# Performance work log

Hardware: AMD Instinct MI355X
Metric: run time of the kernel (lower is better)

Reference implementation:

```python
import jax, jax.numpy as jnp
import numpy as np

B, IN_DIM, D, P = 256, 1024, 512, 2048


def setup_inputs() -> dict:
    key = jax.random.key(0)
    ks = jax.random.split(key, 7)
    return {
        "x": jax.random.normal(ks[0], (B, IN_DIM), dtype=jnp.float32),
        "y": jax.random.randint(ks[1], (B,), 0, P),
        "Wb": jax.random.normal(ks[2], (D, IN_DIM), dtype=jnp.float32) * 0.02,
        "bb": jax.random.normal(ks[3], (D,), dtype=jnp.float32) * 0.02,
        "Wm": jax.random.normal(ks[4], (P, D), dtype=jnp.float32) * 0.02,
        "bm": jax.random.normal(ks[5], (P,), dtype=jnp.float32) * 0.02,
        "proxies": jax.random.normal(ks[6], (P, D), dtype=jnp.float32),
    }


def reference(x, y, Wb, bb, Wm, bm, proxies):
    # backbone: Linear(in_dim -> D)
    feat = x @ Wb.T + bb                         # [B, D]
    # L2-norm regularizer: mean of per-row L2 norms
    reg_e = jnp.mean(jnp.sqrt(jnp.sum(feat * feat, axis=1)))
    # multi: classification head Linear(D -> P)
    out = feat @ Wm.T + bm                       # [B, P]
    # squared euclidean distance to each proxy (broadcast diff + square + sum)
    den = jnp.sum((feat[:, None, :] - proxies[None, :, :]) ** 2, axis=2)  # [B, P]
    # cross-entropy on negated distances
    logp = jax.nn.log_softmax(-den, axis=1)      # [B, P]
    loss = -jnp.mean(jnp.take_along_axis(logp, y[:, None], axis=1))
    return out, loss, reg_e
```

## Files before the change

### kernel.cpp

```cpp
#include <hip/hip_runtime.h>
#include <hip/hip_bf16.h>
#include <math.h>

#define NB   256
#define KIN  1024
#define ND   512
#define NP   2048
#define NTOT 4096

typedef __bf16 bf16x8 __attribute__((ext_vector_type(8)));
typedef float  f32x4  __attribute__((ext_vector_type(4)));
typedef unsigned short ush8 __attribute__((ext_vector_type(8)));

#define OFF_WPB    0u
#define OFF_FEAT32 4194304u
#define OFF_PN2    4718592u
#define OFF_LOGITS 4726784u
#define OFF_ROWLP  6823936u
#define OFF_ROWNM  6824960u

__device__ __forceinline__ ush8 pack8(float4 f0, float4 f1) {
    union { ush8 v; __hip_bfloat162 h[4]; } o;
    o.h[0] = __float22bfloat162_rn(make_float2(f0.x, f0.y));
    o.h[1] = __float22bfloat162_rn(make_float2(f0.z, f0.w));
    o.h[2] = __float22bfloat162_rn(make_float2(f1.x, f1.y));
    o.h[3] = __float22bfloat162_rn(make_float2(f1.z, f1.w));
    return o.v;
}
__device__ __forceinline__ float4 add4(float4 a, float4 b) {
    return make_float4(a.x + b.x, a.y + b.y, a.z + b.z, a.w + b.w);
}

__global__ __launch_bounds__(256) void k_prep(
    const float* __restrict__ Wm, const float* __restrict__ prox,
    unsigned short* __restrict__ WPb, float* __restrict__ pn2,
    float* __restrict__ feat32)
{
    const int t = threadIdx.x, lane = t & 63, w = t >> 6;
    if (t < 128) feat32[blockIdx.x * 128 + t] = 0.f;
    const int r = blockIdx.x * 4 + w;
    const float* src = (r < NP) ? (Wm + (size_t)r * ND)
                                : (prox + (size_t)(r - NP) * ND);
    float4 v0 = *(const float4*)(src + lane * 8);
    float4 v1 = *(const float4*)(src + lane * 8 + 4);
    *(ush8*)(WPb + (size_t)r * ND + lane * 8) = pack8(v0, v1);
    if (r >= NP) {
        float s = v0.x*v0.x + v0.y*v0.y + v0.z*v0.z + v0.w*v0.w
                + v1.x*v1.x + v1.y*v1.y + v1.z*v1.z + v1.w*v1.w;
#pragma unroll
        for (int off = 32; off; off >>= 1) s += __shfl_down(s, off);
        if (lane == 0) pn2[r - NP] = s;
    }
}

__global__ __launch_bounds__(256) void k_feat(
    const float* __restrict__ x, const float* __restrict__ Wb,
    float* __restrict__ feat32)
{
    __shared__ unsigned short As[2][64 * 32];
    __shared__ unsigned short Bs[2][64 * 32];
    const int t = threadIdx.x, lane = t & 63, w = t >> 6;
    const int n0 = blockIdx.x * 64, m0 = blockIdx.y * 64, k0 = blockIdx.z * 128;
    const int srow = t >> 2, sc = (t & 3) * 8;
    const float* gA = x  + (size_t)(m0 + srow) * KIN + k0 + sc;
    const float* gB = Wb + (size_t)(n0 + srow) * KIN + k0 + sc;
    float4 a0 = *(const float4*)gA, a1 = *(const float4*)(gA + 4);
    float4 b0 = *(const float4*)gB, b1 = *(const float4*)(gB + 4);
    f32x4 acc[2][2] = {};
    const int wm = (w >> 1) * 32, wn = (w & 1) * 32;
    const int arow = wm + (lane & 15), brow = wn + (lane & 15);
    const int fcol = (lane >> 4) * 8;
#pragma unroll
    for (int ks = 0; ks < 4; ++ks) {
        *(ush8*)&As[ks & 1][srow * 32 + sc] = pack8(a0, a1);
        *(ush8*)&Bs[ks & 1][srow * 32 + sc] = pack8(b0, b1);
        __syncthreads();
        if (ks + 1 < 4) {
            a0 = *(const float4*)(gA + (ks + 1) * 32);
            a1 = *(const float4*)(gA + (ks + 1) * 32 + 4);
            b0 = *(const float4*)(gB + (ks + 1) * 32);
            b1 = *(const float4*)(gB + (ks + 1) * 32 + 4);
        }
        const unsigned short* as = &As[ks & 1][0];
        const unsigned short* bs = &Bs[ks & 1][0];
        bf16x8 af0 = *(const bf16x8*)&as[(arow     ) * 32 + fcol];
        bf16x8 af1 = *(const bf16x8*)&as[(arow + 16) * 32 + fcol];
        bf16x8 bf0 = *(const bf16x8*)&bs[(brow     ) * 32 + fcol];
        bf16x8 bf1 = *(const bf16x8*)&bs[(brow + 16) * 32 + fcol];
        acc[0][0] = __builtin_amdgcn_mfma_f32_16x16x32_bf16(af0, bf0, acc[0][0], 0, 0, 0);
        acc[0][1] = __builtin_amdgcn_mfma_f32_16x16x32_bf16(af0, bf1, acc[0][1], 0, 0, 0);
        acc[1][0] = __builtin_amdgcn_mfma_f32_16x16x32_bf16(af1, bf0, acc[1][0], 0, 0, 0);
        acc[1][1] = __builtin_amdgcn_mfma_f32_16x16x32_bf16(af1, bf1, acc[1][1], 0, 0, 0);
    }
    const int q = lane >> 4, cn = lane & 15;
#pragma unroll
    for (int i = 0; i < 2; ++i)
#pragma unroll
        for (int j = 0; j < 2; ++j) {
            const int n = n0 + wn + 16 * j + cn;
#pragma unroll
            for (int r = 0; r < 4; ++r) {
                const int m = m0 + wm + 16 * i + q * 4 + r;
                atomicAdd(&feat32[m * ND + n], acc[i][j][r]);
            }
        }
}

__global__ __launch_bounds__(256) void k_head(
    const float* __restrict__ feat32, const float* __restrict__ bb,
    const unsigned short* __restrict__ WPb,
    const float* __restrict__ bm, const float* __restrict__ pn2,
    float* __restrict__ out, float* __restrict__ logits)
{
    __shared__ unsigned short As[2][64 * 32];
    __shared__ unsigned short Bs[2][64 * 32];
    const int t = threadIdx.x, lane = t & 63, w = t >> 6;
    const int n0 = blockIdx.x * 64;
    const int m0 = blockIdx.y * 64;
    const int srow = t >> 2, sc = (t & 3) * 8;
    const float*          gA = feat32 + (size_t)(m0 + srow) * ND + sc;
    const unsigned short* gB = WPb    + (size_t)(n0 + srow) * ND + sc;
    float4 a0 = *(const float4*)gA, a1 = *(const float4*)(gA + 4);
    float4 u0 = *(const float4*)(bb + sc), u1 = *(const float4*)(bb + sc + 4);
    ush8 vb = *(const ush8*)gB;
    f32x4 acc[2][2] = {};
    const int wm = (w >> 1) * 32, wn = (w & 1) * 32;
    const int fr = lane & 15, fcol = (lane >> 4) * 8;
    for (int ks = 0; ks < ND / 32; ++ks) {
        *(ush8*)&As[ks & 1][srow * 32 + sc] = pack8(add4(a0, u0), add4(a1, u1));
        *(ush8*)&Bs[ks & 1][srow * 32 + sc] = vb;
        __syncthreads();
        if (ks + 1 < ND / 32) {
            a0 = *(const float4*)(gA + (ks + 1) * 32);
            a1 = *(const float4*)(gA + (ks + 1) * 32 + 4);
            u0 = *(const float4*)(bb + (ks + 1) * 32 + sc);
            u1 = *(const float4*)(bb + (ks + 1) * 32 + sc + 4);
            vb = *(const ush8*)(gB + (ks + 1) * 32);
        }
        const unsigned short* as = &As[ks & 1][0];
        const unsigned short* bs = &Bs[ks & 1][0];
        bf16x8 af0 = *(const bf16x8*)&as[(wm      + fr) * 32 + fcol];
        bf16x8 af1 = *(const bf16x8*)&as[(wm + 16 + fr) * 32 + fcol];
        bf16x8 bf0 = *(const bf16x8*)&bs[(wn      + fr) * 32 + fcol];
        bf16x8 bf1 = *(const bf16x8*)&bs[(wn + 16 + fr) * 32 + fcol];
        acc[0][0] = __builtin_amdgcn_mfma_f32_16x16x32_bf16(af0, bf0, acc[0][0], 0, 0, 0);
        acc[0][1] = __builtin_amdgcn_mfma_f32_16x16x32_bf16(af0, bf1, acc[0][1], 0, 0, 0);
        acc[1][0] = __builtin_amdgcn_mfma_f32_16x16x32_bf16(af1, bf0, acc[1][0], 0, 0, 0);
        acc[1][1] = __builtin_amdgcn_mfma_f32_16x16x32_bf16(af1, bf1, acc[1][1], 0, 0, 0);
    }
    const bool isProxy = (n0 >= NP);
    const int q = lane >> 4;
#pragma unroll
    for (int i = 0; i < 2; ++i)
#pragma unroll
        for (int j = 0; j < 2; ++j) {
            const int n = n0 + wn + 16 * j + fr;
            const float cadd = isProxy ? pn2[n - NP] : bm[n];
#pragma unroll
            for (int r = 0; r < 4; ++r) {
                const int m = m0 + wm + 16 * i + q * 4 + r;
                const float v = acc[i][j][r];
                if (isProxy) logits[m * NP + (n - NP)] = 2.0f * v - cadd;
                else         out[m * NP + n] = v + cadd;
            }
        }
}

__device__ __forceinline__ float block_reduce(float v, float* sred, int op)
{
    const int lane = threadIdx.x & 63, wave = threadIdx.x >> 6;
#pragma unroll
    for (int off = 32; off; off >>= 1) {
        float o = __shfl_down(v, off);
        v = op ? fmaxf(v, o) : (v + o);
    }
    if (lane == 0) sred[wave] = v;
    __syncthreads();
    if (threadIdx.x == 0) {
        float r = sred[0];
#pragma unroll
        for (int wv = 1; wv < 4; ++wv) r = op ? fmaxf(r, sred[wv]) : (r + sred[wv]);
        sred[0] = r;
    }
    __syncthreads();
    float r = sred[0];
    __syncthreads();
    return r;
}

__global__ __launch_bounds__(256) void k_loss(
    const float* __restrict__ feat32, const float* __restrict__ bb,
    const float* __restrict__ logits, const int* __restrict__ y,
    float* __restrict__ rowlp, float* __restrict__ rownm)
{
    __shared__ float sred[4];
    const int b = blockIdx.x, t = threadIdx.x;

    float v0 = feat32[b * ND + t] + bb[t];
    float v1 = feat32[b * ND + t + 256] + bb[t + 256];
    float fn2 = block_reduce(v0 * v0 + v1 * v1, sred, 0);

    const float* lr = logits + (size_t)b * NP;
    float lv[8], mx = -INFINITY;
#pragma unroll
    for (int j = 0; j < 8; ++j) { lv[j] = lr[t + 256 * j]; mx = fmaxf(mx, lv[j]); }
    float MX = block_reduce(mx, sred, 1);
    float es = 0.f;
#pragma unroll
    for (int j = 0; j < 8; ++j) es += __expf(lv[j] - MX);
    float SUM = block_reduce(es, sred, 0);

    if (t == 0) {
        float ly = lr[y[b]];
        rowlp[b] = ly - MX - __logf(SUM);
        rownm[b] = sqrtf(fn2);
    }
}

__global__ __launch_bounds__(256) void k_final(
    const float* __restrict__ rowlp, const float* __restrict__ rownm,
    float* __restrict__ tail)
{
    __shared__ float sred[4];
    const int t = threadIdx.x;
    float s1 = block_reduce(rowlp[t], sred, 0);
    float s2 = block_reduce(rownm[t], sred, 0);
    if (t == 0) {
        tail[0] = -s1 / (float)NB;
        tail[1] =  s2 / (float)NB;
    }
}

extern "C" void kernel_launch(void* const* d_in, const int* in_sizes, int n_in,
                              void* d_out, int out_size, void* d_ws, size_t ws_size,
                              hipStream_t stream)
{
    const float* x       = (const float*)d_in[0];
    const int*   y       = (const int*)  d_in[1];
    const float* Wb      = (const float*)d_in[2];
    const float* bb      = (const float*)d_in[3];
    const float* Wm      = (const float*)d_in[4];
    const float* bm      = (const float*)d_in[5];
    const float* proxies = (const float*)d_in[6];

    char* ws = (char*)d_ws;
    unsigned short* WPb    = (unsigned short*)(ws + OFF_WPB);
    float*          feat32 = (float*)(ws + OFF_FEAT32);
    float*          pn2    = (float*)(ws + OFF_PN2);
    float*          logits = (float*)(ws + OFF_LOGITS);
    float*          rowlp  = (float*)(ws + OFF_ROWLP);
    float*          rownm  = (float*)(ws + OFF_ROWNM);

    float* out  = (float*)d_out;
    float* tail = out + (size_t)NB * NP;

    k_prep <<<dim3(NTOT / 4), dim3(256), 0, stream>>>(Wm, proxies, WPb, pn2, feat32);
    k_feat <<<dim3(ND / 64, NB / 64, 8), dim3(256), 0, stream>>>(x, Wb, feat32);
    k_head <<<dim3(NTOT / 64, NB / 64), dim3(256), 0, stream>>>(
        feat32, bb, WPb, bm, pn2, out, logits);
    k_loss <<<dim3(NB), dim3(256), 0, stream>>>(feat32, bb, logits, y, rowlp, rownm);
    k_final<<<dim3(1), dim3(256), 0, stream>>>(rowlp, rownm, tail);
}
```

Before: 97.31 us.

## Halve GEMM N-tiles for more blocks and fold final reduction into loss kernel

The N tile width in both the feature GEMM and the head GEMM drops from 64 to 32 columns. This doubles the grid so more of the GPU's compute units are busy on these small matrices. The separate one-block final reduction kernel is removed. Instead, each loss block atomically accumulates its row log-prob and norm, and the last block to arrive, found via an agent-scope counter, writes the means. This saves one kernel launch, at the cost of reloading the A tile twice as often and making the float sums order-nondeterministic.

```diff
diff --git a/kernel.cpp b/kernel.cpp
--- a/kernel.cpp
+++ b/kernel.cpp
@@ -11,13 +11,13 @@
 typedef __bf16 bf16x8 __attribute__((ext_vector_type(8)));
 typedef float  f32x4  __attribute__((ext_vector_type(4)));
 typedef unsigned short ush8 __attribute__((ext_vector_type(8)));
+typedef unsigned short ush4 __attribute__((ext_vector_type(4)));
 
 #define OFF_WPB    0u
 #define OFF_FEAT32 4194304u
 #define OFF_PN2    4718592u
 #define OFF_LOGITS 4726784u
-#define OFF_ROWLP  6823936u
-#define OFF_ROWNM  6824960u
+#define OFF_SYNC   6823936u
 
 __device__ __forceinline__ ush8 pack8(float4 f0, float4 f1) {
     union { ush8 v; __hip_bfloat162 h[4]; } o;
@@ -27,6 +27,12 @@
     o.h[3] = __float22bfloat162_rn(make_float2(f1.z, f1.w));
     return o.v;
 }
+__device__ __forceinline__ ush4 pack4(float4 f) {
+    union { ush4 v; __hip_bfloat162 h[2]; } o;
+    o.h[0] = __float22bfloat162_rn(make_float2(f.x, f.y));
+    o.h[1] = __float22bfloat162_rn(make_float2(f.z, f.w));
+    return o.v;
+}
 __device__ __forceinline__ float4 add4(float4 a, float4 b) {
     return make_float4(a.x + b.x, a.y + b.y, a.z + b.z, a.w + b.w);
 }
@@ -34,10 +40,15 @@
 __global__ __launch_bounds__(256) void k_prep(
     const float* __restrict__ Wm, const float* __restrict__ prox,
     unsigned short* __restrict__ WPb, float* __restrict__ pn2,
-    float* __restrict__ feat32)
+    float* __restrict__ feat32, unsigned* __restrict__ sync_area)
 {
     const int t = threadIdx.x, lane = t & 63, w = t >> 6;
     if (t < 128) feat32[blockIdx.x * 128 + t] = 0.f;
+    if (blockIdx.x == 0 && t == 0) {
+        sync_area[0] = 0u;
+        ((float*)sync_area)[4] = 0.f;
+        ((float*)sync_area)[5] = 0.f;
+    }
     const int r = blockIdx.x * 4 + w;
     const float* src = (r < NP) ? (Wm + (size_t)r * ND)
                                 : (prox + (size_t)(r - NP) * ND);
@@ -58,51 +69,44 @@
     float* __restrict__ feat32)
 {
     __shared__ unsigned short As[2][64 * 32];
-    __shared__ unsigned short Bs[2][64 * 32];
+    __shared__ unsigned short Bs[2][32 * 32];
     const int t = threadIdx.x, lane = t & 63, w = t >> 6;
-    const int n0 = blockIdx.x * 64, m0 = blockIdx.y * 64, k0 = blockIdx.z * 128;
-    const int srow = t >> 2, sc = (t & 3) * 8;
-    const float* gA = x  + (size_t)(m0 + srow) * KIN + k0 + sc;
-    const float* gB = Wb + (size_t)(n0 + srow) * KIN + k0 + sc;
+    const int n0 = blockIdx.x * 32, m0 = blockIdx.y * 64, k0 = blockIdx.z * 128;
+    const int sar = t >> 2, sac = (t & 3) * 8;
+    const int sbr = t >> 3, sbc = (t & 7) * 4;
+    const float* gA = x  + (size_t)(m0 + sar) * KIN + k0 + sac;
+    const float* gB = Wb + (size_t)(n0 + sbr) * KIN + k0 + sbc;
     float4 a0 = *(const float4*)gA, a1 = *(const float4*)(gA + 4);
-    float4 b0 = *(const float4*)gB, b1 = *(const float4*)(gB + 4);
-    f32x4 acc[2][2] = {};
-    const int wm = (w >> 1) * 32, wn = (w & 1) * 32;
-    const int arow = wm + (lane & 15), brow = wn + (lane & 15);
-    const int fcol = (lane >> 4) * 8;
+    float4 b0 = *(const float4*)gB;
+    f32x4 acc[2] = {};
+    const int wm = (w >> 1) * 32, wn = (w & 1) * 16;
+    const int fr = lane & 15, fcol = (lane >> 4) * 8;
 #pragma unroll
     for (int ks = 0; ks < 4; ++ks) {
-        *(ush8*)&As[ks & 1][srow * 32 + sc] = pack8(a0, a1);
-        *(ush8*)&Bs[ks & 1][srow * 32 + sc] = pack8(b0, b1);
+        *(ush8*)&As[ks & 1][sar * 32 + sac] = pack8(a0, a1);
+        *(ush4*)&Bs[ks & 1][sbr * 32 + sbc] = pack4(b0);
         __syncthreads();
         if (ks + 1 < 4) {
             a0 = *(const float4*)(gA + (ks + 1) * 32);
             a1 = *(const float4*)(gA + (ks + 1) * 32 + 4);
             b0 = *(const float4*)(gB + (ks + 1) * 32);
-            b1 = *(const float4*)(gB + (ks + 1) * 32 + 4);
         }
         const unsigned short* as = &As[ks & 1][0];
         const unsigned short* bs = &Bs[ks & 1][0];
-        bf16x8 af0 = *(const bf16x8*)&as[(arow     ) * 32 + fcol];
-        bf16x8 af1 = *(const bf16x8*)&as[(arow + 16) * 32 + fcol];
-        bf16x8 bf0 = *(const bf16x8*)&bs[(brow     ) * 32 + fcol];
-        bf16x8 bf1 = *(const bf16x8*)&bs[(brow + 16) * 32 + fcol];
-        acc[0][0] = __builtin_amdgcn_mfma_f32_16x16x32_bf16(af0, bf0, acc[0][0], 0, 0, 0);
-        acc[0][1] = __builtin_amdgcn_mfma_f32_16x16x32_bf16(af0, bf1, acc[0][1], 0, 0, 0);
-        acc[1][0] = __builtin_amdgcn_mfma_f32_16x16x32_bf16(af1, bf0, acc[1][0], 0, 0, 0);
-        acc[1][1] = __builtin_amdgcn_mfma_f32_16x16x32_bf16(af1, bf1, acc[1][1], 0, 0, 0);
+        bf16x8 af0 = *(const bf16x8*)&as[(wm      + fr) * 32 + fcol];
+        bf16x8 af1 = *(const bf16x8*)&as[(wm + 16 + fr) * 32 + fcol];
+        bf16x8 bf  = *(const bf16x8*)&bs[(wn      + fr) * 32 + fcol];
+        acc[0] = __builtin_amdgcn_mfma_f32_16x16x32_bf16(af0, bf, acc[0], 0, 0, 0);
+        acc[1] = __builtin_amdgcn_mfma_f32_16x16x32_bf16(af1, bf, acc[1], 0, 0, 0);
     }
     const int q = lane >> 4, cn = lane & 15;
+    const int n = n0 + wn + cn;
 #pragma unroll
     for (int i = 0; i < 2; ++i)
 #pragma unroll
-        for (int j = 0; j < 2; ++j) {
-            const int n = n0 + wn + 16 * j + cn;
-#pragma unroll
-            for (int r = 0; r < 4; ++r) {
-                const int m = m0 + wm + 16 * i + q * 4 + r;
-                atomicAdd(&feat32[m * ND + n], acc[i][j][r]);
-            }
+        for (int r = 0; r < 4; ++r) {
+            const int m = m0 + wm + 16 * i + q * 4 + r;
+            atomicAdd(&feat32[m * ND + n], acc[i][r]);
         }
 }
 
@@ -113,56 +117,51 @@
     float* __restrict__ out, float* __restrict__ logits)
 {
     __shared__ unsigned short As[2][64 * 32];
-    __shared__ unsigned short Bs[2][64 * 32];
+    __shared__ unsigned short Bs[2][32 * 32];
     const int t = threadIdx.x, lane = t & 63, w = t >> 6;
-    const int n0 = blockIdx.x * 64;
+    const int n0 = blockIdx.x * 32;
     const int m0 = blockIdx.y * 64;
-    const int srow = t >> 2, sc = (t & 3) * 8;
-    const float*          gA = feat32 + (size_t)(m0 + srow) * ND + sc;
-    const unsigned short* gB = WPb    + (size_t)(n0 + srow) * ND + sc;
+    const int sar = t >> 2, sac = (t & 3) * 8;
+    const int sbr = t >> 3, sbc = (t & 7) * 4;
+    const float*          gA = feat32 + (size_t)(m0 + sar) * ND + sac;
+    const unsigned short* gB = WPb    + (size_t)(n0 + sbr) * ND + sbc;
     float4 a0 = *(const float4*)gA, a1 = *(const float4*)(gA + 4);
-    float4 u0 = *(const float4*)(bb + sc), u1 = *(const float4*)(bb + sc + 4);
-    ush8 vb = *(const ush8*)gB;
-    f32x4 acc[2][2] = {};
-    const int wm = (w >> 1) * 32, wn = (w & 1) * 32;
+    float4 u0 = *(const float4*)(bb + sac), u1 = *(const float4*)(bb + sac + 4);
+    ush4 vb = *(const ush4*)gB;
+    f32x4 acc[2] = {};
+    const int wm = (w >> 1) * 32, wn = (w & 1) * 16;
     const int fr = lane & 15, fcol = (lane >> 4) * 8;
     for (int ks = 0; ks < ND / 32; ++ks) {
-        *(ush8*)&As[ks & 1][srow * 32 + sc] = pack8(add4(a0, u0), add4(a1, u1));
-        *(ush8*)&Bs[ks & 1][srow * 32 + sc] = vb;
+        *(ush8*)&As[ks & 1][sar * 32 + sac] = pack8(add4(a0, u0), add4(a1, u1));
+        *(ush4*)&Bs[ks & 1][sbr * 32 + sbc] = vb;
         __syncthreads();
         if (ks + 1 < ND / 32) {
             a0 = *(const float4*)(gA + (ks + 1) * 32);
             a1 = *(const float4*)(gA + (ks + 1) * 32 + 4);
-            u0 = *(const float4*)(bb + (ks + 1) * 32 + sc);
-            u1 = *(const float4*)(bb + (ks + 1) * 32 + sc + 4);
-            vb = *(const ush8*)(gB + (ks + 1) * 32);
+            u0 = *(const float4*)(bb + (ks + 1) * 32 + sac);
+            u1 = *(const float4*)(bb + (ks + 1) * 32 + sac + 4);
+            vb = *(const ush4*)(gB + (ks + 1) * 32);
         }
         const unsigned short* as = &As[ks & 1][0];
         const unsigned short* bs = &Bs[ks & 1][0];
         bf16x8 af0 = *(const bf16x8*)&as[(wm      + fr) * 32 + fcol];
         bf16x8 af1 = *(const bf16x8*)&as[(wm + 16 + fr) * 32 + fcol];
-        bf16x8 bf0 = *(const bf16x8*)&bs[(wn      + fr) * 32 + fcol];
-        bf16x8 bf1 = *(const bf16x8*)&bs[(wn + 16 + fr) * 32 + fcol];
-        acc[0][0] = __builtin_amdgcn_mfma_f32_16x16x32_bf16(af0, bf0, acc[0][0], 0, 0, 0);
-        acc[0][1] = __builtin_amdgcn_mfma_f32_16x16x32_bf16(af0, bf1, acc[0][1], 0, 0, 0);
-        acc[1][0] = __builtin_amdgcn_mfma_f32_16x16x32_bf16(af1, bf0, acc[1][0], 0, 0, 0);
-        acc[1][1] = __builtin_amdgcn_mfma_f32_16x16x32_bf16(af1, bf1, acc[1][1], 0, 0, 0);
+        bf16x8 bf  = *(const bf16x8*)&bs[(wn      + fr) * 32 + fcol];
+        acc[0] = __builtin_amdgcn_mfma_f32_16x16x32_bf16(af0, bf, acc[0], 0, 0, 0);
+        acc[1] = __builtin_amdgcn_mfma_f32_16x16x32_bf16(af1, bf, acc[1], 0, 0, 0);
     }
     const bool isProxy = (n0 >= NP);
-    const int q = lane >> 4;
+    const int q = lane >> 4, cn = lane & 15;
+    const int n = n0 + wn + cn;
+    const float cadd = isProxy ? pn2[n - NP] : bm[n];
 #pragma unroll
     for (int i = 0; i < 2; ++i)
 #pragma unroll
-        for (int j = 0; j < 2; ++j) {
-            const int n = n0 + wn + 16 * j + fr;
-            const float cadd = isProxy ? pn2[n - NP] : bm[n];
-#pragma unroll
-            for (int r = 0; r < 4; ++r) {
-                const int m = m0 + wm + 16 * i + q * 4 + r;
-                const float v = acc[i][j][r];
-                if (isProxy) logits[m * NP + (n - NP)] = 2.0f * v - cadd;
-                else         out[m * NP + n] = v + cadd;
-            }
+        for (int r = 0; r < 4; ++r) {
+            const int m = m0 + wm + 16 * i + q * 4 + r;
+            const float v = acc[i][r];
+            if (isProxy) logits[m * NP + (n - NP)] = 2.0f * v - cadd;
+            else         out[m * NP + n] = v + cadd;
         }
 }
 
@@ -191,7 +190,7 @@
 __global__ __launch_bounds__(256) void k_loss(
     const float* __restrict__ feat32, const float* __restrict__ bb,
     const float* __restrict__ logits, const int* __restrict__ y,
-    float* __restrict__ rowlp, float* __restrict__ rownm)
+    unsigned* __restrict__ sync_area, float* __restrict__ tail)
 {
     __shared__ float sred[4];
     const int b = blockIdx.x, t = threadIdx.x;
@@ -211,23 +210,17 @@
     float SUM = block_reduce(es, sred, 0);
 
     if (t == 0) {
-        float ly = lr[y[b]];
-        rowlp[b] = ly - MX - __logf(SUM);
-        rownm[b] = sqrtf(fn2);
-    }
-}
-
-__global__ __launch_bounds__(256) void k_final(
-    const float* __restrict__ rowlp, const float* __restrict__ rownm,
-    float* __restrict__ tail)
-{
-    __shared__ float sred[4];
-    const int t = threadIdx.x;
-    float s1 = block_reduce(rowlp[t], sred, 0);
-    float s2 = block_reduce(rownm[t], sred, 0);
-    if (t == 0) {
-        tail[0] = -s1 / (float)NB;
-        tail[1] =  s2 / (float)NB;
+        float* accum = (float*)sync_area + 4;
+        atomicAdd(&accum[0], lr[y[b]] - MX - __logf(SUM));
+        atomicAdd(&accum[1], sqrtf(fn2));
+        unsigned old = __hip_atomic_fetch_add(&sync_area[0], 1u,
+                           __ATOMIC_ACQ_REL, __HIP_MEMORY_SCOPE_AGENT);
+        if (old == NB - 1) {
+            float s0 = __hip_atomic_load(&accum[0], __ATOMIC_RELAXED, __HIP_MEMORY_SCOPE_AGENT);
+            float s1 = __hip_atomic_load(&accum[1], __ATOMIC_RELAXED, __HIP_MEMORY_SCOPE_AGENT);
+            tail[0] = -s0 / (float)NB;
+            tail[1] =  s1 / (float)NB;
+        }
     }
 }
 
@@ -248,16 +241,14 @@
     float*          feat32 = (float*)(ws + OFF_FEAT32);
     float*          pn2    = (float*)(ws + OFF_PN2);
     float*          logits = (float*)(ws + OFF_LOGITS);
-    float*          rowlp  = (float*)(ws + OFF_ROWLP);
-    float*          rownm  = (float*)(ws + OFF_ROWNM);
+    unsigned*       sync_a = (unsigned*)(ws + OFF_SYNC);
 
     float* out  = (float*)d_out;
     float* tail = out + (size_t)NB * NP;
 
-    k_prep <<<dim3(NTOT / 4), dim3(256), 0, stream>>>(Wm, proxies, WPb, pn2, feat32);
-    k_feat <<<dim3(ND / 64, NB / 64, 8), dim3(256), 0, stream>>>(x, Wb, feat32);
-    k_head <<<dim3(NTOT / 64, NB / 64), dim3(256), 0, stream>>>(
+    k_prep<<<dim3(NTOT / 4), dim3(256), 0, stream>>>(Wm, proxies, WPb, pn2, feat32, sync_a);
+    k_feat<<<dim3(ND / 32, NB / 64, 8), dim3(256), 0, stream>>>(x, Wb, feat32);
+    k_head<<<dim3(NTOT / 32, NB / 64), dim3(256), 0, stream>>>(
         feat32, bb, WPb, bm, pn2, out, logits);
-    k_loss <<<dim3(NB), dim3(256), 0, stream>>>(feat32, bb, logits, y, rowlp, rownm);
-    k_final<<<dim3(1), dim3(256), 0, stream>>>(rowlp, rownm, tail);
-}
+    k_loss<<<dim3(NB), dim3(256), 0, stream>>>(feat32, bb, logits, y, sync_a, tail);
+}
```

New measurement: 104.7 us. 1.08x slower.

## Fuse weight conversion into head GEMM and final reduction into loss kernel

Applied to the files above, without the earlier changes.

Removes the separate prep kernel that converted Wm and proxies to bf16 and computed proxy norms. The head GEMM now loads fp32 weights directly, packs them to bf16 while staging into shared memory, and accumulates the proxy squared norms in-kernel. The final reduction kernel is replaced by atomics plus a last-block-done counter in the loss kernel, and zeroing moves to a memset. This cuts two launches and the bf16 round trip through memory, but each of the four row-block tiles now reads fp32 weights at twice the bytes, redoing the conversion per tile.

```diff
diff --git a/kernel.cpp b/kernel.cpp
--- a/kernel.cpp
+++ b/kernel.cpp
@@ -12,12 +12,9 @@
 typedef float  f32x4  __attribute__((ext_vector_type(4)));
 typedef unsigned short ush8 __attribute__((ext_vector_type(8)));
 
-#define OFF_WPB    0u
-#define OFF_FEAT32 4194304u
-#define OFF_PN2    4718592u
-#define OFF_LOGITS 4726784u
-#define OFF_ROWLP  6823936u
-#define OFF_ROWNM  6824960u
+#define OFF_FEAT32 0u
+#define OFF_SYNC   524288u
+#define OFF_LOGITS 524416u
 
 __device__ __forceinline__ ush8 pack8(float4 f0, float4 f1) {
     union { ush8 v; __hip_bfloat162 h[4]; } o;
@@ -29,28 +26,6 @@
 }
 __device__ __forceinline__ float4 add4(float4 a, float4 b) {
     return make_float4(a.x + b.x, a.y + b.y, a.z + b.z, a.w + b.w);
-}
-
-__global__ __launch_bounds__(256) void k_prep(
-    const float* __restrict__ Wm, const float* __restrict__ prox,
-    unsigned short* __restrict__ WPb, float* __restrict__ pn2,
-    float* __restrict__ feat32)
-{
-    const int t = threadIdx.x, lane = t & 63, w = t >> 6;
-    if (t < 128) feat32[blockIdx.x * 128 + t] = 0.f;
-    const int r = blockIdx.x * 4 + w;
-    const float* src = (r < NP) ? (Wm + (size_t)r * ND)
-                                : (prox + (size_t)(r - NP) * ND);
-    float4 v0 = *(const float4*)(src + lane * 8);
-    float4 v1 = *(const float4*)(src + lane * 8 + 4);
-    *(ush8*)(WPb + (size_t)r * ND + lane * 8) = pack8(v0, v1);
-    if (r >= NP) {
-        float s = v0.x*v0.x + v0.y*v0.y + v0.z*v0.z + v0.w*v0.w
-                + v1.x*v1.x + v1.y*v1.y + v1.z*v1.z + v1.w*v1.w;
-#pragma unroll
-        for (int off = 32; off; off >>= 1) s += __shfl_down(s, off);
-        if (lane == 0) pn2[r - NP] = s;
-    }
 }
 
 __global__ __launch_bounds__(256) void k_feat(
@@ -108,34 +83,43 @@
 
 __global__ __launch_bounds__(256) void k_head(
     const float* __restrict__ feat32, const float* __restrict__ bb,
-    const unsigned short* __restrict__ WPb,
-    const float* __restrict__ bm, const float* __restrict__ pn2,
-    float* __restrict__ out, float* __restrict__ logits)
+    const float* __restrict__ Wm, const float* __restrict__ prox,
+    const float* __restrict__ bm, float* __restrict__ out,
+    float* __restrict__ logits)
 {
     __shared__ unsigned short As[2][64 * 32];
     __shared__ unsigned short Bs[2][64 * 32];
+    __shared__ float pn2s[64];
     const int t = threadIdx.x, lane = t & 63, w = t >> 6;
     const int n0 = blockIdx.x * 64;
     const int m0 = blockIdx.y * 64;
+    const bool isProxy = (n0 >= NP);
+    const float* Bsrc = isProxy ? (prox + (size_t)(n0 - NP) * ND)
+                                : (Wm   + (size_t)n0 * ND);
     const int srow = t >> 2, sc = (t & 3) * 8;
-    const float*          gA = feat32 + (size_t)(m0 + srow) * ND + sc;
-    const unsigned short* gB = WPb    + (size_t)(n0 + srow) * ND + sc;
+    const float* gA = feat32 + (size_t)(m0 + srow) * ND + sc;
+    const float* gB = Bsrc   + (size_t)srow * ND + sc;
     float4 a0 = *(const float4*)gA, a1 = *(const float4*)(gA + 4);
     float4 u0 = *(const float4*)(bb + sc), u1 = *(const float4*)(bb + sc + 4);
-    ush8 vb = *(const ush8*)gB;
+    float4 b0 = *(const float4*)gB, b1 = *(const float4*)(gB + 4);
     f32x4 acc[2][2] = {};
+    float ssum = 0.f;
     const int wm = (w >> 1) * 32, wn = (w & 1) * 32;
     const int fr = lane & 15, fcol = (lane >> 4) * 8;
     for (int ks = 0; ks < ND / 32; ++ks) {
         *(ush8*)&As[ks & 1][srow * 32 + sc] = pack8(add4(a0, u0), add4(a1, u1));
-        *(ush8*)&Bs[ks & 1][srow * 32 + sc] = vb;
+        *(ush8*)&Bs[ks & 1][srow * 32 + sc] = pack8(b0, b1);
+        if (isProxy)
+            ssum += b0.x*b0.x + b0.y*b0.y + b0.z*b0.z + b0.w*b0.w
+                  + b1.x*b1.x + b1.y*b1.y + b1.z*b1.z + b1.w*b1.w;
         __syncthreads();
         if (ks + 1 < ND / 32) {
             a0 = *(const float4*)(gA + (ks + 1) * 32);
             a1 = *(const float4*)(gA + (ks + 1) * 32 + 4);
             u0 = *(const float4*)(bb + (ks + 1) * 32 + sc);
             u1 = *(const float4*)(bb + (ks + 1) * 32 + sc + 4);
-            vb = *(const ush8*)(gB + (ks + 1) * 32);
+            b0 = *(const float4*)(gB + (ks + 1) * 32);
+            b1 = *(const float4*)(gB + (ks + 1) * 32 + 4);
         }
         const unsigned short* as = &As[ks & 1][0];
         const unsigned short* bs = &Bs[ks & 1][0];
@@ -148,14 +132,20 @@
         acc[1][0] = __builtin_amdgcn_mfma_f32_16x16x32_bf16(af1, bf0, acc[1][0], 0, 0, 0);
         acc[1][1] = __builtin_amdgcn_mfma_f32_16x16x32_bf16(af1, bf1, acc[1][1], 0, 0, 0);
     }
-    const bool isProxy = (n0 >= NP);
+    if (isProxy) {
+        ssum += __shfl_xor(ssum, 1);
+        ssum += __shfl_xor(ssum, 2);
+        if ((t & 3) == 0) pn2s[srow] = ssum;
+    }
+    __syncthreads();
     const int q = lane >> 4;
 #pragma unroll
     for (int i = 0; i < 2; ++i)
 #pragma unroll
         for (int j = 0; j < 2; ++j) {
-            const int n = n0 + wn + 16 * j + fr;
-            const float cadd = isProxy ? pn2[n - NP] : bm[n];
+            const int nl = wn + 16 * j + fr;
+            const int n = n0 + nl;
+            const float cadd = isProxy ? pn2s[nl] : bm[n];
 #pragma unroll
             for (int r = 0; r < 4; ++r) {
                 const int m = m0 + wm + 16 * i + q * 4 + r;
@@ -191,7 +181,7 @@
 __global__ __launch_bounds__(256) void k_loss(
     const float* __restrict__ feat32, const float* __restrict__ bb,
     const float* __restrict__ logits, const int* __restrict__ y,
-    float* __restrict__ rowlp, float* __restrict__ rownm)
+    unsigned* __restrict__ sync_area, float* __restrict__ tail)
 {
     __shared__ float sred[4];
     const int b = blockIdx.x, t = threadIdx.x;
@@ -211,23 +201,17 @@
     float SUM = block_reduce(es, sred, 0);
 
     if (t == 0) {
-        float ly = lr[y[b]];
-        rowlp[b] = ly - MX - __logf(SUM);
-        rownm[b] = sqrtf(fn2);
-    }
-}
-
-__global__ __launch_bounds__(256) void k_final(
-    const float* __restrict__ rowlp, const float* __restrict__ rownm,
-    float* __restrict__ tail)
-{
-    __shared__ float sred[4];
-    const int t = threadIdx.x;
-    float s1 = block_reduce(rowlp[t], sred, 0);
-    float s2 = block_reduce(rownm[t], sred, 0);
-    if (t == 0) {
-        tail[0] = -s1 / (float)NB;
-        tail[1] =  s2 / (float)NB;
+        float* accum = (float*)sync_area + 4;
+        atomicAdd(&accum[0], lr[y[b]] - MX - __logf(SUM));
+        atomicAdd(&accum[1], sqrtf(fn2));
+        unsigned old = __hip_atomic_fetch_add(&sync_area[0], 1u,
+                           __ATOMIC_ACQ_REL, __HIP_MEMORY_SCOPE_AGENT);
+        if (old == NB - 1) {
+            float s0 = __hip_atomic_load(&accum[0], __ATOMIC_RELAXED, __HIP_MEMORY_SCOPE_AGENT);
+            float s1 = __hip_atomic_load(&accum[1], __ATOMIC_RELAXED, __HIP_MEMORY_SCOPE_AGENT);
+            tail[0] = -s0 / (float)NB;
+            tail[1] =  s1 / (float)NB;
+        }
     }
 }
 
@@ -244,20 +228,16 @@
     const float* proxies = (const float*)d_in[6];
 
     char* ws = (char*)d_ws;
-    unsigned short* WPb    = (unsigned short*)(ws + OFF_WPB);
-    float*          feat32 = (float*)(ws + OFF_FEAT32);
-    float*          pn2    = (float*)(ws + OFF_PN2);
-    float*          logits = (float*)(ws + OFF_LOGITS);
-    float*          rowlp  = (float*)(ws + OFF_ROWLP);
-    float*          rownm  = (float*)(ws + OFF_ROWNM);
+    float*    feat32 = (float*)(ws + OFF_FEAT32);
+    unsigned* sync_a = (unsigned*)(ws + OFF_SYNC);
+    float*    logits = (float*)(ws + OFF_LOGITS);
 
     float* out  = (float*)d_out;
     float* tail = out + (size_t)NB * NP;
 
-    k_prep <<<dim3(NTOT / 4), dim3(256), 0, stream>>>(Wm, proxies, WPb, pn2, feat32);
-    k_feat <<<dim3(ND / 64, NB / 64, 8), dim3(256), 0, stream>>>(x, Wb, feat32);
-    k_head <<<dim3(NTOT / 64, NB / 64), dim3(256), 0, stream>>>(
-        feat32, bb, WPb, bm, pn2, out, logits);
-    k_loss <<<dim3(NB), dim3(256), 0, stream>>>(feat32, bb, logits, y, rowlp, rownm);
-    k_final<<<dim3(1), dim3(256), 0, stream>>>(rowlp, rownm, tail);
-}
+    hipMemsetAsync(ws + OFF_FEAT32, 0, 524288u + 128u, stream);
+    k_feat<<<dim3(ND / 64, NB / 64, 8), dim3(256), 0, stream>>>(x, Wb, feat32);
+    k_head<<<dim3(NTOT / 64, NB / 64), dim3(256), 0, stream>>>(
+        feat32, bb, Wm, proxies, bm, out, logits);
+    k_loss<<<dim3(NB), dim3(256), 0, stream>>>(feat32, bb, logits, y, sync_a, tail);
+}
```

Result: slower. 107.8 us (+10.8%).

## Merge prep and feat kernels, fold final reduction into loss via atomics

Applied to the files above, without the earlier changes.

Merges the weight-conversion prep kernel and the split-K backbone GEMM into one launch with block-index dispatch, and replaces the zeroing of feat32 with a hipMemsetAsync that also clears a sync/accumulator area. The separate final reduction kernel is removed. Each loss block now atomically adds its per-row log-prob and norm and bumps a counter, and the last block writes the two scalar outputs. This cuts launch count and lets prep and GEMM blocks run concurrently, at the cost of a memset node and float atomics that make the sum order nondeterministic.

```diff
diff --git a/kernel.cpp b/kernel.cpp
--- a/kernel.cpp
+++ b/kernel.cpp
@@ -12,12 +12,11 @@
 typedef float  f32x4  __attribute__((ext_vector_type(4)));
 typedef unsigned short ush8 __attribute__((ext_vector_type(8)));
 
-#define OFF_WPB    0u
-#define OFF_FEAT32 4194304u
-#define OFF_PN2    4718592u
-#define OFF_LOGITS 4726784u
-#define OFF_ROWLP  6823936u
-#define OFF_ROWNM  6824960u
+#define OFF_FEAT32 0u
+#define OFF_SYNC   524288u
+#define OFF_WPB    524416u
+#define OFF_PN2    4718720u
+#define OFF_LOGITS 4726912u
 
 __device__ __forceinline__ ush8 pack8(float4 f0, float4 f1) {
     union { ush8 v; __hip_bfloat162 h[4]; } o;
@@ -31,79 +30,78 @@
     return make_float4(a.x + b.x, a.y + b.y, a.z + b.z, a.w + b.w);
 }
 
-__global__ __launch_bounds__(256) void k_prep(
+__global__ __launch_bounds__(256) void k_one(
+    const float* __restrict__ x, const float* __restrict__ Wb,
     const float* __restrict__ Wm, const float* __restrict__ prox,
-    unsigned short* __restrict__ WPb, float* __restrict__ pn2,
-    float* __restrict__ feat32)
-{
-    const int t = threadIdx.x, lane = t & 63, w = t >> 6;
-    if (t < 128) feat32[blockIdx.x * 128 + t] = 0.f;
-    const int r = blockIdx.x * 4 + w;
-    const float* src = (r < NP) ? (Wm + (size_t)r * ND)
-                                : (prox + (size_t)(r - NP) * ND);
-    float4 v0 = *(const float4*)(src + lane * 8);
-    float4 v1 = *(const float4*)(src + lane * 8 + 4);
-    *(ush8*)(WPb + (size_t)r * ND + lane * 8) = pack8(v0, v1);
-    if (r >= NP) {
-        float s = v0.x*v0.x + v0.y*v0.y + v0.z*v0.z + v0.w*v0.w
-                + v1.x*v1.x + v1.y*v1.y + v1.z*v1.z + v1.w*v1.w;
-#pragma unroll
-        for (int off = 32; off; off >>= 1) s += __shfl_down(s, off);
-        if (lane == 0) pn2[r - NP] = s;
-    }
-}
-
-__global__ __launch_bounds__(256) void k_feat(
-    const float* __restrict__ x, const float* __restrict__ Wb,
-    float* __restrict__ feat32)
-{
-    __shared__ unsigned short As[2][64 * 32];
-    __shared__ unsigned short Bs[2][64 * 32];
-    const int t = threadIdx.x, lane = t & 63, w = t >> 6;
-    const int n0 = blockIdx.x * 64, m0 = blockIdx.y * 64, k0 = blockIdx.z * 128;
-    const int srow = t >> 2, sc = (t & 3) * 8;
-    const float* gA = x  + (size_t)(m0 + srow) * KIN + k0 + sc;
-    const float* gB = Wb + (size_t)(n0 + srow) * KIN + k0 + sc;
-    float4 a0 = *(const float4*)gA, a1 = *(const float4*)(gA + 4);
-    float4 b0 = *(const float4*)gB, b1 = *(const float4*)(gB + 4);
-    f32x4 acc[2][2] = {};
-    const int wm = (w >> 1) * 32, wn = (w & 1) * 32;
-    const int arow = wm + (lane & 15), brow = wn + (lane & 15);
-    const int fcol = (lane >> 4) * 8;
-#pragma unroll
-    for (int ks = 0; ks < 4; ++ks) {
-        *(ush8*)&As[ks & 1][srow * 32 + sc] = pack8(a0, a1);
-        *(ush8*)&Bs[ks & 1][srow * 32 + sc] = pack8(b0, b1);
-        __syncthreads();
-        if (ks + 1 < 4) {
-            a0 = *(const float4*)(gA + (ks + 1) * 32);
-            a1 = *(const float4*)(gA + (ks + 1) * 32 + 4);
-            b0 = *(const float4*)(gB + (ks + 1) * 32);
-            b1 = *(const float4*)(gB + (ks + 1) * 32 + 4);
-        }
-        const unsigned short* as = &As[ks & 1][0];
-        const unsigned short* bs = &Bs[ks & 1][0];
-        bf16x8 af0 = *(const bf16x8*)&as[(arow     ) * 32 + fcol];
-        bf16x8 af1 = *(const bf16x8*)&as[(arow + 16) * 32 + fcol];
-        bf16x8 bf0 = *(const bf16x8*)&bs[(brow     ) * 32 + fcol];
-        bf16x8 bf1 = *(const bf16x8*)&bs[(brow + 16) * 32 + fcol];
-        acc[0][0] = __builtin_amdgcn_mfma_f32_16x16x32_bf16(af0, bf0, acc[0][0], 0, 0, 0);
-        acc[0][1] = __builtin_amdgcn_mfma_f32_16x16x32_bf16(af0, bf1, acc[0][1], 0, 0, 0);
-        acc[1][0] = __builtin_amdgcn_mfma_f32_16x16x32_bf16(af1, bf0, acc[1][0], 0, 0, 0);
-        acc[1][1] = __builtin_amdgcn_mfma_f32_16x16x32_bf16(af1, bf1, acc[1][1], 0, 0, 0);
-    }
-    const int q = lane >> 4, cn = lane & 15;
-#pragma unroll
-    for (int i = 0; i < 2; ++i)
-#pragma unroll
-        for (int j = 0; j < 2; ++j) {
-            const int n = n0 + wn + 16 * j + cn;
-#pragma unroll
-            for (int r = 0; r < 4; ++r) {
-                const int m = m0 + wm + 16 * i + q * 4 + r;
-                atomicAdd(&feat32[m * ND + n], acc[i][j][r]);
+    float* __restrict__ feat32, unsigned short* __restrict__ WPb,
+    float* __restrict__ pn2)
+{
+    const int bid = blockIdx.x, t = threadIdx.x;
+    const int lane = t & 63, w = t >> 6;
+    if (bid < 256) {
+        __shared__ unsigned short As[2][64 * 32];
+        __shared__ unsigned short Bs[2][64 * 32];
+        const int n0 = (bid & 7) * 64;
+        const int m0 = ((bid >> 3) & 3) * 64;
+        const int k0 = (bid >> 5) * 128;
+        const int srow = t >> 2, sc = (t & 3) * 8;
+        const float* gA = x  + (size_t)(m0 + srow) * KIN + k0 + sc;
+        const float* gB = Wb + (size_t)(n0 + srow) * KIN + k0 + sc;
+        float4 a0 = *(const float4*)gA, a1 = *(const float4*)(gA + 4);
+        float4 b0 = *(const float4*)gB, b1 = *(const float4*)(gB + 4);
+        f32x4 acc[2][2] = {};
+        const int wm = (w >> 1) * 32, wn = (w & 1) * 32;
+        const int arow = wm + (lane & 15), brow = wn + (lane & 15);
+        const int fcol = (lane >> 4) * 8;
+#pragma unroll
+        for (int ks = 0; ks < 4; ++ks) {
+            *(ush8*)&As[ks & 1][srow * 32 + sc] = pack8(a0, a1);
+            *(ush8*)&Bs[ks & 1][srow * 32 + sc] = pack8(b0, b1);
+            __syncthreads();
+            if (ks + 1 < 4) {
+                a0 = *(const float4*)(gA + (ks + 1) * 32);
+                a1 = *(const float4*)(gA + (ks + 1) * 32 + 4);
+                b0 = *(const float4*)(gB + (ks + 1) * 32);
+                b1 = *(const float4*)(gB + (ks + 1) * 32 + 4);
             }
-        }
+            const unsigned short* as = &As[ks & 1][0];
+            const unsigned short* bs = &Bs[ks & 1][0];
+            bf16x8 af0 = *(const bf16x8*)&as[(arow     ) * 32 + fcol];
+            bf16x8 af1 = *(const bf16x8*)&as[(arow + 16) * 32 + fcol];
+            bf16x8 bf0 = *(const bf16x8*)&bs[(brow     ) * 32 + fcol];
+            bf16x8 bf1 = *(const bf16x8*)&bs[(brow + 16) * 32 + fcol];
+            acc[0][0] = __builtin_amdgcn_mfma_f32_16x16x32_bf16(af0, bf0, acc[0][0], 0, 0, 0);
+            acc[0][1] = __builtin_amdgcn_mfma_f32_16x16x32_bf16(af0, bf1, acc[0][1], 0, 0, 0);
+            acc[1][0] = __builtin_amdgcn_mfma_f32_16x16x32_bf16(af1, bf0, acc[1][0], 0, 0, 0);
+            acc[1][1] = __builtin_amdgcn_mfma_f32_16x16x32_bf16(af1, bf1, acc[1][1], 0, 0, 0);
+        }
+        const int q = lane >> 4, cn = lane & 15;
+#pragma unroll
+        for (int i = 0; i < 2; ++i)
+#pragma unroll
+            for (int j = 0; j < 2; ++j) {
+                const int n = n0 + wn + 16 * j + cn;
+#pragma unroll
+                for (int r = 0; r < 4; ++r) {
+                    const int m = m0 + wm + 16 * i + q * 4 + r;
+                    atomicAdd(&feat32[m * ND + n], acc[i][j][r]);
+                }
+            }
+    } else {
+        const int r = (bid - 256) * 4 + w;
+        const float* src = (r < NP) ? (Wm + (size_t)r * ND)
+                                    : (prox + (size_t)(r - NP) * ND);
+        float4 v0 = *(const float4*)(src + lane * 8);
+        float4 v1 = *(const float4*)(src + lane * 8 + 4);
+        *(ush8*)(WPb + (size_t)r * ND + lane * 8) = pack8(v0, v1);
+        if (r >= NP) {
+            float s = v0.x*v0.x + v0.y*v0.y + v0.z*v0.z + v0.w*v0.w
+                    + v1.x*v1.x + v1.y*v1.y + v1.z*v1.z + v1.w*v1.w;
+#pragma unroll
+            for (int off = 32; off; off >>= 1) s += __shfl_down(s, off);
+            if (lane == 0) pn2[r - NP] = s;
+        }
+    }
 }
 
 __global__ __launch_bounds__(256) void k_head(
@@ -191,7 +189,7 @@
 __global__ __launch_bounds__(256) void k_loss(
     const float* __restrict__ feat32, const float* __restrict__ bb,
     const float* __restrict__ logits, const int* __restrict__ y,
-    float* __restrict__ rowlp, float* __restrict__ rownm)
+    unsigned* __restrict__ sync_area, float* __restrict__ tail)
 {
     __shared__ float sred[4];
     const int b = blockIdx.x, t = threadIdx.x;
@@ -211,23 +209,17 @@
     float SUM = block_reduce(es, sred, 0);
 
     if (t == 0) {
-        float ly = lr[y[b]];
-        rowlp[b] = ly - MX - __logf(SUM);
-        rownm[b] = sqrtf(fn2);
-    }
-}
-
-__global__ __launch_bounds__(256) void k_final(
-    const float* __restrict__ rowlp, const float* __restrict__ rownm,
-    float* __restrict__ tail)
-{
-    __shared__ float sred[4];
-    const int t = threadIdx.x;
-    float s1 = block_reduce(rowlp[t], sred, 0);
-    float s2 = block_reduce(rownm[t], sred, 0);
-    if (t == 0) {
-        tail[0] = -s1 / (float)NB;
-        tail[1] =  s2 / (float)NB;
+        float* accum = (float*)sync_area + 4;
+        atomicAdd(&accum[0], lr[y[b]] - MX - __logf(SUM));
+        atomicAdd(&accum[1], sqrtf(fn2));
+        unsigned old = __hip_atomic_fetch_add(&sync_area[0], 1u,
+                           __ATOMIC_ACQ_REL, __HIP_MEMORY_SCOPE_AGENT);
+        if (old == NB - 1) {
+            float s0 = __hip_atomic_load(&accum[0], __ATOMIC_RELAXED, __HIP_MEMORY_SCOPE_AGENT);
+            float s1 = __hip_atomic_load(&accum[1], __ATOMIC_RELAXED, __HIP_MEMORY_SCOPE_AGENT);
+            tail[0] = -s0 / (float)NB;
+            tail[1] =  s1 / (float)NB;
+        }
     }
 }
 
@@ -244,20 +236,19 @@
     const float* proxies = (const float*)d_in[6];
 
     char* ws = (char*)d_ws;
+    float*          feat32 = (float*)(ws + OFF_FEAT32);
+    unsigned*       sync_a = (unsigned*)(ws + OFF_SYNC);
     unsigned short* WPb    = (unsigned short*)(ws + OFF_WPB);
-    float*          feat32 = (float*)(ws + OFF_FEAT32);
     float*          pn2    = (float*)(ws + OFF_PN2);
     float*          logits = (float*)(ws + OFF_LOGITS);
-    float*          rowlp  = (float*)(ws + OFF_ROWLP);
-    float*          rownm  = (float*)(ws + OFF_ROWNM);
 
     float* out  = (float*)d_out;
     float* tail = out + (size_t)NB * NP;
 
-    k_prep <<<dim3(NTOT / 4), dim3(256), 0, stream>>>(Wm, proxies, WPb, pn2, feat32);
-    k_feat <<<dim3(ND / 64, NB / 64, 8), dim3(256), 0, stream>>>(x, Wb, feat32);
-    k_head <<<dim3(NTOT / 64, NB / 64), dim3(256), 0, stream>>>(
+    hipMemsetAsync(ws + OFF_FEAT32, 0, 524288u + 128u, stream);
+    k_one <<<dim3(1280), dim3(256), 0, stream>>>(
+        x, Wb, Wm, proxies, feat32, WPb, pn2);
+    k_head<<<dim3(NTOT / 64, NB / 64), dim3(256), 0, stream>>>(
         feat32, bb, WPb, bm, pn2, out, logits);
-    k_loss <<<dim3(NB), dim3(256), 0, stream>>>(feat32, bb, logits, y, rowlp, rownm);
-    k_final<<<dim3(1), dim3(256), 0, stream>>>(rowlp, rownm, tail);
-}
+    k_loss<<<dim3(NB), dim3(256), 0, stream>>>(feat32, bb, logits, y, sync_a, tail);
+}
```

Result: slower. 104.7 us (+7.6%).
